# Kernel tuning notes

Hardware: AMD Instinct MI355X
Metric: run time of the kernel (lower is better)

Reference implementation:

```python
import jax, jax.numpy as jnp
import numpy as np

N_NODES = 2048
N_GRAPHS = 64
N_EDGES = 16384
B = 65536
META = 64
TX = 8
NOISE = 128
IN_DIM = N_NODES + 1 + 32 + TX  # 2089


def setup_inputs() -> dict:
    key = jax.random.key(0)
    ks = jax.random.split(key, 11)
    return {
        "batched_graphs": jax.random.randint(ks[0], (B,), 0, N_GRAPHS),
        "batched_chain": jax.random.normal(ks[1], (B,), dtype=jnp.float32),
        "trigger_data": jax.random.normal(ks[2], (B, META), dtype=jnp.float32),
        "tx_start_time": jax.random.normal(ks[3], (B, TX), dtype=jnp.float32),
        "edges": jax.random.randint(ks[4], (N_GRAPHS, 2, N_EDGES), 0, N_NODES),
        "gcn_w": jax.random.normal(ks[5], (), dtype=jnp.float32),
        "gcn_b": jax.random.normal(ks[6], (), dtype=jnp.float32) * 0.01,
        "trig_W": jax.random.normal(ks[7], (META, 32), dtype=jnp.float32) / np.sqrt(META),
        "trig_b": jnp.zeros((32,), dtype=jnp.float32),
        "emb_W": jax.random.normal(ks[8], (IN_DIM, NOISE), dtype=jnp.float32) / np.sqrt(IN_DIM),
        "emb_b": jnp.zeros((NOISE,), dtype=jnp.float32),
    }


def _gcn_one_graph(edge_index, w, b):
    # GCNConv(1,1) on x = ones(n_nodes,1): add self loops, sym-normalize.
    self_idx = jnp.arange(N_NODES, dtype=edge_index.dtype)
    src = jnp.concatenate([edge_index[0], self_idx])
    dst = jnp.concatenate([edge_index[1], self_idx])
    deg = jax.ops.segment_sum(jnp.ones(src.shape[0], jnp.float32), dst,
                              num_segments=N_NODES)
    dinv = jnp.where(deg > 0, jax.lax.rsqrt(deg), 0.0)
    norm = dinv[src] * dinv[dst]
    agg = jax.ops.segment_sum(norm, dst, num_segments=N_NODES)  # [n_nodes]
    return agg * w + b  # x @ W with x==1 is just w per node, plus bias


def reference(batched_graphs, batched_chain, trigger_data, tx_start_time,
              edges, gcn_w, gcn_b, trig_W, trig_b, emb_W, emb_b):
    # Per-graph GCN embeddings for all topologies (covers all uniques). [G, n_nodes]
    graph_emb = jax.vmap(lambda e: _gcn_one_graph(e, gcn_w, gcn_b))(edges)
    ge = graph_emb[batched_graphs]                         # [B, n_nodes] gather
    trig = jax.nn.relu(trigger_data @ trig_W + trig_b)     # [B, 32]
    x = jnp.concatenate(
        [ge, batched_chain[:, None], trig, tx_start_time], axis=1)  # [B, IN_DIM]
    return x @ emb_W + emb_b                               # [B, NOISE]
```

## Files before the change

### kernel.cpp

```cpp
#include <hip/hip_runtime.h>

#define NN 2048
#define NG 64
#define NE 16384
#define BB 65536
#define META 64
#define TXD 8
#define NOISE 128


__global__ __launch_bounds__(256) void agg_kernel(
    const int* __restrict__ edges,
    const float* __restrict__ gcn_w,
    const float* __restrict__ gcn_b,
    float* __restrict__ emb,
    float* __restrict__ graph_out)
{
    __shared__ int                s_cnt[NN];
    __shared__ float              s_dinv[NN];
    __shared__ unsigned long long s_acc[NN];
    const int g = blockIdx.x, tid = threadIdx.x;
    const int4* __restrict__ e4 = (const int4*)(edges + (size_t)g * 2 * NE);

    if (tid < NOISE) graph_out[g * NOISE + tid] = 0.0f;

    int4 ds[16];
    #pragma unroll
    for (int k = 0; k < 16; ++k) ds[k] = e4[4096 + k * 256 + tid];

    for (int n = tid; n < NN; n += 256) { s_cnt[n] = 1; s_acc[n] = 0ull; }
    __syncthreads();

    #pragma unroll
    for (int k = 0; k < 16; ++k) {
        atomicAdd(&s_cnt[ds[k].x], 1);
        atomicAdd(&s_cnt[ds[k].y], 1);
        atomicAdd(&s_cnt[ds[k].z], 1);
        atomicAdd(&s_cnt[ds[k].w], 1);
    }
    __syncthreads();
    for (int n = tid; n < NN; n += 256) s_dinv[n] = rsqrtf((float)s_cnt[n]);
    __syncthreads();

    const float SCALE = 1099511627776.0f;
    #pragma unroll
    for (int k = 0; k < 16; ++k) {
        int4 sr = e4[k * 256 + tid];
        float nx = s_dinv[sr.x] * s_dinv[ds[k].x];
        float ny = s_dinv[sr.y] * s_dinv[ds[k].y];
        float nz = s_dinv[sr.z] * s_dinv[ds[k].z];
        float nw = s_dinv[sr.w] * s_dinv[ds[k].w];
        atomicAdd(&s_acc[ds[k].x], (unsigned long long)(nx * SCALE));
        atomicAdd(&s_acc[ds[k].y], (unsigned long long)(ny * SCALE));
        atomicAdd(&s_acc[ds[k].z], (unsigned long long)(nz * SCALE));
        atomicAdd(&s_acc[ds[k].w], (unsigned long long)(nw * SCALE));
    }
    __syncthreads();

    const float w = gcn_w[0], b = gcn_b[0];
    for (int n = tid; n < NN; n += 256) {
        float di = s_dinv[n];
        float agg = (float)((double)s_acc[n] * 0x1p-40) + di * di;
        emb[(size_t)g * NN + n] = agg * w + b;
    }
}

__global__ __launch_bounds__(256) void fold_kernel(
    const float* __restrict__ emb,
    const float* __restrict__ emb_W,
    float* __restrict__ graph_out)
{
    __shared__ float s_e[128];
    __shared__ float s_red[128];
    const int tid = threadIdx.x;
    const int g = blockIdx.x >> 4, chunk = blockIdx.x & 15;
    const int n0 = chunk * 128;
    if (tid < 128) s_e[tid] = emb[(size_t)g * NN + n0 + tid];
    __syncthreads();
    const int c = tid & 127, h = tid >> 7;
    const float* __restrict__ Wp = emb_W + (size_t)(n0 + h * 64) * NOISE + c;
    const float* __restrict__ ep = s_e + h * 64;
    float a0 = 0.f, a1 = 0.f, a2 = 0.f, a3 = 0.f;
    #pragma unroll
    for (int i = 0; i < 64; i += 4) {
        a0 = fmaf(ep[i + 0], Wp[(i + 0) * NOISE], a0);
        a1 = fmaf(ep[i + 1], Wp[(i + 1) * NOISE], a1);
        a2 = fmaf(ep[i + 2], Wp[(i + 2) * NOISE], a2);
        a3 = fmaf(ep[i + 3], Wp[(i + 3) * NOISE], a3);
    }
    float acc = (a0 + a1) + (a2 + a3);
    if (h == 1) s_red[c] = acc;
    __syncthreads();
    if (h == 0) atomicAdd(&graph_out[g * NOISE + c], acc + s_red[c]);
}

#define ROWS 32
__global__ __launch_bounds__(256, 3) void main_kernel(
    const int* __restrict__ bg,
    const float* __restrict__ chain,
    const float* __restrict__ trig_in,
    const float* __restrict__ txs,
    const float* __restrict__ trig_W,
    const float* __restrict__ trig_b,
    const float* __restrict__ emb_W,
    const float* __restrict__ emb_b,
    const float* __restrict__ graph_out,
    float* __restrict__ out)
{
    __shared__ float s_td[ROWS * 68];
    __shared__ float s_twT[32 * 68];
    __shared__ float s_trig[ROWS * 36];
    __shared__ float s_tx[ROWS * TXD];
    __shared__ float s_ch[ROWS];
    __shared__ int   s_gi[ROWS];

    const int tid = threadIdx.x;
    const int row0 = blockIdx.x * ROWS;

    {
        const float4* __restrict__ gsrc =
            (const float4*)(trig_in + (size_t)row0 * META);
        #pragma unroll
        for (int k = 0; k < 2; ++k) {
            int t = tid + k * 256;
            int r = t >> 4, i4 = t & 15;
            *(float4*)&s_td[r * 68 + i4 * 4] = gsrc[t];
        }
    }
    {
        const float4* __restrict__ gsrc = (const float4*)trig_W;
        #pragma unroll
        for (int k = 0; k < 2; ++k) {
            int t = tid + k * 256;
            int i = t >> 3, j4 = (t & 7) * 4;
            float4 v = gsrc[t];
            s_twT[(j4 + 0) * 68 + i] = v.x;
            s_twT[(j4 + 1) * 68 + i] = v.y;
            s_twT[(j4 + 2) * 68 + i] = v.z;
            s_twT[(j4 + 3) * 68 + i] = v.w;
        }
    }
    if (tid < 64) {
        int r = tid >> 1, k4 = (tid & 1) * 4;
        *(float4*)&s_tx[r * TXD + k4] =
            ((const float4*)(txs + (size_t)row0 * TXD))[tid];
    } else if (tid < 96) {
        int r = tid - 64;
        s_ch[r] = chain[row0 + r];
    } else if (tid < 128) {
        int r = tid - 96;
        s_gi[r] = bg[row0 + r];
    }

    const int n0 = (tid & 63) * 2;
    float2 w2[32], w3[TXD];
    #pragma unroll
    for (int j = 0; j < 32; ++j)
        w2[j] = *(const float2*)&emb_W[(size_t)(2049 + j) * NOISE + n0];
    #pragma unroll
    for (int k = 0; k < TXD; ++k)
        w3[k] = *(const float2*)&emb_W[(size_t)(2081 + k) * NOISE + n0];
    const float2 w1   = *(const float2*)&emb_W[(size_t)2048 * NOISE + n0];
    const float2 bias = *(const float2*)&emb_b[n0];

    __syncthreads();

    {
        const int j0 = tid & 15;
        const int r0 = (tid >> 4) * 2;
        const float* __restrict__ tw0 = s_twT + j0 * 68;
        const float* __restrict__ tw1 = s_twT + (j0 + 16) * 68;
        const float* __restrict__ td0 = s_td + r0 * 68;
        const float* __restrict__ td1 = s_td + (r0 + 1) * 68;
        float b0 = trig_b[j0], b1 = trig_b[j0 + 16];
        float a00 = b0, a01 = b1, a10 = b0, a11 = b1;
        #pragma unroll
        for (int i = 0; i < META; i += 4) {
            float4 u0 = *(const float4*)(tw0 + i);
            float4 u1 = *(const float4*)(tw1 + i);
            float4 t0 = *(const float4*)(td0 + i);
            float4 t1 = *(const float4*)(td1 + i);
            a00 = fmaf(t0.x, u0.x, a00); a00 = fmaf(t0.y, u0.y, a00);
            a00 = fmaf(t0.z, u0.z, a00); a00 = fmaf(t0.w, u0.w, a00);
            a01 = fmaf(t0.x, u1.x, a01); a01 = fmaf(t0.y, u1.y, a01);
            a01 = fmaf(t0.z, u1.z, a01); a01 = fmaf(t0.w, u1.w, a01);
            a10 = fmaf(t1.x, u0.x, a10); a10 = fmaf(t1.y, u0.y, a10);
            a10 = fmaf(t1.z, u0.z, a10); a10 = fmaf(t1.w, u0.w, a10);
            a11 = fmaf(t1.x, u1.x, a11); a11 = fmaf(t1.y, u1.y, a11);
            a11 = fmaf(t1.z, u1.z, a11); a11 = fmaf(t1.w, u1.w, a11);
        }
        s_trig[r0 * 36 + j0]            = fmaxf(a00, 0.f);
        s_trig[r0 * 36 + j0 + 16]       = fmaxf(a01, 0.f);
        s_trig[(r0 + 1) * 36 + j0]      = fmaxf(a10, 0.f);
        s_trig[(r0 + 1) * 36 + j0 + 16] = fmaxf(a11, 0.f);
    }
    __syncthreads();

    const int wv = tid >> 6;
    int   gs[8];
    float chs[8];
    #pragma unroll
    for (int p = 0; p < 8; ++p) {
        const int r = p * 4 + wv;
        gs[p]  = s_gi[r];
        chs[p] = s_ch[r];
    }
    float2 go[8];
    #pragma unroll
    for (int p = 0; p < 8; ++p)
        go[p] = *(const float2*)&graph_out[gs[p] * NOISE + n0];

    #pragma unroll
    for (int p = 0; p < 8; ++p) {
        const int r = p * 4 + wv;
        const int row = row0 + r;
        float ax = bias.x + go[p].x + chs[p] * w1.x;
        float ay = bias.y + go[p].y + chs[p] * w1.y;
        const float4* __restrict__ tx4 = (const float4*)(s_tx + r * TXD);
        float4 t0 = tx4[0], t1 = tx4[1];
        ax = fmaf(t0.x, w3[0].x, ax); ay = fmaf(t0.x, w3[0].y, ay);
        ax = fmaf(t0.y, w3[1].x, ax); ay = fmaf(t0.y, w3[1].y, ay);
        ax = fmaf(t0.z, w3[2].x, ax); ay = fmaf(t0.z, w3[2].y, ay);
        ax = fmaf(t0.w, w3[3].x, ax); ay = fmaf(t0.w, w3[3].y, ay);
        ax = fmaf(t1.x, w3[4].x, ax); ay = fmaf(t1.x, w3[4].y, ay);
        ax = fmaf(t1.y, w3[5].x, ax); ay = fmaf(t1.y, w3[5].y, ay);
        ax = fmaf(t1.z, w3[6].x, ax); ay = fmaf(t1.z, w3[6].y, ay);
        ax = fmaf(t1.w, w3[7].x, ax); ay = fmaf(t1.w, w3[7].y, ay);
        const float* __restrict__ tg = s_trig + r * 36;
        #pragma unroll
        for (int q = 0; q < 8; ++q) {
            float4 t4 = *(const float4*)(tg + q * 4);
            ax = fmaf(t4.x, w2[4 * q + 0].x, ax); ay = fmaf(t4.x, w2[4 * q + 0].y, ay);
            ax = fmaf(t4.y, w2[4 * q + 1].x, ax); ay = fmaf(t4.y, w2[4 * q + 1].y, ay);
            ax = fmaf(t4.z, w2[4 * q + 2].x, ax); ay = fmaf(t4.z, w2[4 * q + 2].y, ay);
            ax = fmaf(t4.w, w2[4 * q + 3].x, ax); ay = fmaf(t4.w, w2[4 * q + 3].y, ay);
        }
        *(float2*)&out[(size_t)row * NOISE + n0] = make_float2(ax, ay);
    }
}

extern "C" void kernel_launch(void* const* d_in, const int* in_sizes, int n_in,
                              void* d_out, int out_size, void* d_ws, size_t ws_size,
                              hipStream_t stream) {
    const int*   bg      = (const int*)d_in[0];
    const float* chain   = (const float*)d_in[1];
    const float* trig_in = (const float*)d_in[2];
    const float* txs     = (const float*)d_in[3];
    const int*   edges   = (const int*)d_in[4];
    const float* gcn_w   = (const float*)d_in[5];
    const float* gcn_b   = (const float*)d_in[6];
    const float* trig_W  = (const float*)d_in[7];
    const float* trig_b  = (const float*)d_in[8];
    const float* emb_W   = (const float*)d_in[9];
    const float* emb_b   = (const float*)d_in[10];
    float* out = (float*)d_out;

    float* graph_out = (float*)d_ws;
    float* emb       = (float*)d_ws + NG * NOISE;

    agg_kernel<<<NG, 256, 0, stream>>>(edges, gcn_w, gcn_b, emb, graph_out);
    fold_kernel<<<NG * 16, 256, 0, stream>>>(emb, emb_W, graph_out);
    main_kernel<<<BB / ROWS, 256, 0, stream>>>(bg, chain, trig_in, txs, trig_W,
                                               trig_b, emb_W, emb_b, graph_out, out);
}
```

Baseline: 128.2 us.

## Split per-graph GCN aggregation across four blocks and slim main kernel registers

The single 64-block aggregation kernel becomes two kernels of 256 blocks each. A degree pass writes per-quarter partial counts and an accumulation pass reads them, and the fold kernel now sums those partials to build the node embeddings. This spreads the serial edge work across more CUs, at the cost of an extra launch and more workspace traffic. The main kernel also drops its shared staging of trig_W, tx, chain and graph indices and reads them directly, loads the emb_W trigger rows per q-step instead of holding them in registers, and raises the occupancy hint to 4 blocks per CU.

```diff
diff --git a/kernel.cpp b/kernel.cpp
--- a/kernel.cpp
+++ b/kernel.cpp
@@ -9,64 +9,90 @@
 #define NOISE 128
 
 
-__global__ __launch_bounds__(256) void agg_kernel(
+__global__ __launch_bounds__(256) void deg_kernel(
     const int* __restrict__ edges,
+    const float* __restrict__ trig_W,
+    int* __restrict__ deg4,
+    float* __restrict__ twT,
+    float* __restrict__ graph_out)
+{
+    __shared__ int s_cnt[NN];
+    const int tid = threadIdx.x;
+    const int g = blockIdx.x >> 2, q = blockIdx.x & 3;
+
+    for (int n = tid; n < NN; n += 256) s_cnt[n] = 0;
+
+    if (q == 0 && tid < NOISE) graph_out[g * NOISE + tid] = 0.0f;
+    if (blockIdx.x == 1) {
+        for (int idx = tid; idx < META * 32; idx += 256) {
+            int i = idx >> 5, j = idx & 31;
+            twT[j * META + i] = trig_W[idx];
+        }
+    }
+    __syncthreads();
+
+    const int4* __restrict__ ed =
+        (const int4*)(edges + ((size_t)g * 2 + 1) * NE + q * 4096);
+    #pragma unroll
+    for (int k = 0; k < 4; ++k) {
+        int4 d = ed[k * 256 + tid];
+        atomicAdd(&s_cnt[d.x], 1);
+        atomicAdd(&s_cnt[d.y], 1);
+        atomicAdd(&s_cnt[d.z], 1);
+        atomicAdd(&s_cnt[d.w], 1);
+    }
+    __syncthreads();
+
+    int* __restrict__ dst = deg4 + (size_t)blockIdx.x * NN;
+    for (int n = tid; n < NN; n += 256) dst[n] = s_cnt[n];
+}
+
+__global__ __launch_bounds__(256) void acc_kernel(
+    const int* __restrict__ edges,
+    const int* __restrict__ deg4,
+    float* __restrict__ acc4)
+{
+    __shared__ float              s_dinv[NN];
+    __shared__ unsigned long long s_acc[NN];
+    const int tid = threadIdx.x;
+    const int g = blockIdx.x >> 2, q = blockIdx.x & 3;
+
+    for (int n = tid; n < NN; n += 256) {
+        int d = deg4[((size_t)g * 4 + 0) * NN + n]
+              + deg4[((size_t)g * 4 + 1) * NN + n]
+              + deg4[((size_t)g * 4 + 2) * NN + n]
+              + deg4[((size_t)g * 4 + 3) * NN + n] + 1;
+        s_dinv[n] = rsqrtf((float)d);
+        s_acc[n] = 0ull;
+    }
+    __syncthreads();
+
+    const int4* __restrict__ es =
+        (const int4*)(edges + (size_t)g * 2 * NE + q * 4096);
+    const int4* __restrict__ ed =
+        (const int4*)(edges + ((size_t)g * 2 + 1) * NE + q * 4096);
+    const float SCALE = 1099511627776.0f;
+    #pragma unroll
+    for (int k = 0; k < 4; ++k) {
+        int4 s = es[k * 256 + tid];
+        int4 d = ed[k * 256 + tid];
+        atomicAdd(&s_acc[d.x], (unsigned long long)(s_dinv[s.x] * s_dinv[d.x] * SCALE));
+        atomicAdd(&s_acc[d.y], (unsigned long long)(s_dinv[s.y] * s_dinv[d.y] * SCALE));
+        atomicAdd(&s_acc[d.z], (unsigned long long)(s_dinv[s.z] * s_dinv[d.z] * SCALE));
+        atomicAdd(&s_acc[d.w], (unsigned long long)(s_dinv[s.w] * s_dinv[d.w] * SCALE));
+    }
+    __syncthreads();
+
+    float* __restrict__ dst = acc4 + (size_t)blockIdx.x * NN;
+    for (int n = tid; n < NN; n += 256)
+        dst[n] = (float)((double)s_acc[n] * 0x1p-40);
+}
+
+__global__ __launch_bounds__(256) void fold_kernel(
+    const int* __restrict__ deg4,
+    const float* __restrict__ acc4,
     const float* __restrict__ gcn_w,
     const float* __restrict__ gcn_b,
-    float* __restrict__ emb,
-    float* __restrict__ graph_out)
-{
-    __shared__ int                s_cnt[NN];
-    __shared__ float              s_dinv[NN];
-    __shared__ unsigned long long s_acc[NN];
-    const int g = blockIdx.x, tid = threadIdx.x;
-    const int4* __restrict__ e4 = (const int4*)(edges + (size_t)g * 2 * NE);
-
-    if (tid < NOISE) graph_out[g * NOISE + tid] = 0.0f;
-
-    int4 ds[16];
-    #pragma unroll
-    for (int k = 0; k < 16; ++k) ds[k] = e4[4096 + k * 256 + tid];
-
-    for (int n = tid; n < NN; n += 256) { s_cnt[n] = 1; s_acc[n] = 0ull; }
-    __syncthreads();
-
-    #pragma unroll
-    for (int k = 0; k < 16; ++k) {
-        atomicAdd(&s_cnt[ds[k].x], 1);
-        atomicAdd(&s_cnt[ds[k].y], 1);
-        atomicAdd(&s_cnt[ds[k].z], 1);
-        atomicAdd(&s_cnt[ds[k].w], 1);
-    }
-    __syncthreads();
-    for (int n = tid; n < NN; n += 256) s_dinv[n] = rsqrtf((float)s_cnt[n]);
-    __syncthreads();
-
-    const float SCALE = 1099511627776.0f;
-    #pragma unroll
-    for (int k = 0; k < 16; ++k) {
-        int4 sr = e4[k * 256 + tid];
-        float nx = s_dinv[sr.x] * s_dinv[ds[k].x];
-        float ny = s_dinv[sr.y] * s_dinv[ds[k].y];
-        float nz = s_dinv[sr.z] * s_dinv[ds[k].z];
-        float nw = s_dinv[sr.w] * s_dinv[ds[k].w];
-        atomicAdd(&s_acc[ds[k].x], (unsigned long long)(nx * SCALE));
-        atomicAdd(&s_acc[ds[k].y], (unsigned long long)(ny * SCALE));
-        atomicAdd(&s_acc[ds[k].z], (unsigned long long)(nz * SCALE));
-        atomicAdd(&s_acc[ds[k].w], (unsigned long long)(nw * SCALE));
-    }
-    __syncthreads();
-
-    const float w = gcn_w[0], b = gcn_b[0];
-    for (int n = tid; n < NN; n += 256) {
-        float di = s_dinv[n];
-        float agg = (float)((double)s_acc[n] * 0x1p-40) + di * di;
-        emb[(size_t)g * NN + n] = agg * w + b;
-    }
-}
-
-__global__ __launch_bounds__(256) void fold_kernel(
-    const float* __restrict__ emb,
     const float* __restrict__ emb_W,
     float* __restrict__ graph_out)
 {
@@ -75,7 +101,19 @@
     const int tid = threadIdx.x;
     const int g = blockIdx.x >> 4, chunk = blockIdx.x & 15;
     const int n0 = chunk * 128;
-    if (tid < 128) s_e[tid] = emb[(size_t)g * NN + n0 + tid];
+    if (tid < 128) {
+        const int n = n0 + tid;
+        int d = deg4[((size_t)g * 4 + 0) * NN + n]
+              + deg4[((size_t)g * 4 + 1) * NN + n]
+              + deg4[((size_t)g * 4 + 2) * NN + n]
+              + deg4[((size_t)g * 4 + 3) * NN + n] + 1;
+        float di = rsqrtf((float)d);
+        float a = acc4[((size_t)g * 4 + 0) * NN + n]
+                + acc4[((size_t)g * 4 + 1) * NN + n]
+                + acc4[((size_t)g * 4 + 2) * NN + n]
+                + acc4[((size_t)g * 4 + 3) * NN + n] + di * di;
+        s_e[tid] = a * gcn_w[0] + gcn_b[0];
+    }
     __syncthreads();
     const int c = tid & 127, h = tid >> 7;
     const float* __restrict__ Wp = emb_W + (size_t)(n0 + h * 64) * NOISE + c;
@@ -95,24 +133,20 @@
 }
 
 #define ROWS 32
-__global__ __launch_bounds__(256, 3) void main_kernel(
+__global__ __launch_bounds__(256, 4) void main_kernel(
     const int* __restrict__ bg,
     const float* __restrict__ chain,
     const float* __restrict__ trig_in,
     const float* __restrict__ txs,
-    const float* __restrict__ trig_W,
     const float* __restrict__ trig_b,
+    const float* __restrict__ twT,
     const float* __restrict__ emb_W,
     const float* __restrict__ emb_b,
     const float* __restrict__ graph_out,
     float* __restrict__ out)
 {
     __shared__ float s_td[ROWS * 68];
-    __shared__ float s_twT[32 * 68];
     __shared__ float s_trig[ROWS * 36];
-    __shared__ float s_tx[ROWS * TXD];
-    __shared__ float s_ch[ROWS];
-    __shared__ int   s_gi[ROWS];
 
     const int tid = threadIdx.x;
     const int row0 = blockIdx.x * ROWS;
@@ -127,52 +161,26 @@
             *(float4*)&s_td[r * 68 + i4 * 4] = gsrc[t];
         }
     }
-    {
-        const float4* __restrict__ gsrc = (const float4*)trig_W;
-        #pragma unroll
-        for (int k = 0; k < 2; ++k) {
-            int t = tid + k * 256;
-            int i = t >> 3, j4 = (t & 7) * 4;
-            float4 v = gsrc[t];
-            s_twT[(j4 + 0) * 68 + i] = v.x;
-            s_twT[(j4 + 1) * 68 + i] = v.y;
-            s_twT[(j4 + 2) * 68 + i] = v.z;
-            s_twT[(j4 + 3) * 68 + i] = v.w;
-        }
-    }
-    if (tid < 64) {
-        int r = tid >> 1, k4 = (tid & 1) * 4;
-        *(float4*)&s_tx[r * TXD + k4] =
-            ((const float4*)(txs + (size_t)row0 * TXD))[tid];
-    } else if (tid < 96) {
-        int r = tid - 64;
-        s_ch[r] = chain[row0 + r];
-    } else if (tid < 128) {
-        int r = tid - 96;
-        s_gi[r] = bg[row0 + r];
-    }
 
     const int n0 = (tid & 63) * 2;
-    float2 w2[32], w3[TXD];
-    #pragma unroll
-    for (int j = 0; j < 32; ++j)
-        w2[j] = *(const float2*)&emb_W[(size_t)(2049 + j) * NOISE + n0];
+    float2 w3[TXD];
     #pragma unroll
     for (int k = 0; k < TXD; ++k)
         w3[k] = *(const float2*)&emb_W[(size_t)(2081 + k) * NOISE + n0];
     const float2 w1   = *(const float2*)&emb_W[(size_t)2048 * NOISE + n0];
     const float2 bias = *(const float2*)&emb_b[n0];
 
+    const int j0 = tid & 15;
+    const int r0 = (tid >> 4) * 2;
+    const float b0 = trig_b[j0], b1 = trig_b[j0 + 16];
+
     __syncthreads();
 
     {
-        const int j0 = tid & 15;
-        const int r0 = (tid >> 4) * 2;
-        const float* __restrict__ tw0 = s_twT + j0 * 68;
-        const float* __restrict__ tw1 = s_twT + (j0 + 16) * 68;
+        const float* __restrict__ tw0 = twT + j0 * META;
+        const float* __restrict__ tw1 = twT + (j0 + 16) * META;
         const float* __restrict__ td0 = s_td + r0 * 68;
         const float* __restrict__ td1 = s_td + (r0 + 1) * 68;
-        float b0 = trig_b[j0], b1 = trig_b[j0 + 16];
         float a00 = b0, a01 = b1, a10 = b0, a11 = b1;
         #pragma unroll
         for (int i = 0; i < META; i += 4) {
@@ -197,27 +205,19 @@
     __syncthreads();
 
     const int wv = tid >> 6;
-    int   gs[8];
-    float chs[8];
-    #pragma unroll
-    for (int p = 0; p < 8; ++p) {
-        const int r = p * 4 + wv;
-        gs[p]  = s_gi[r];
-        chs[p] = s_ch[r];
-    }
-    float2 go[8];
-    #pragma unroll
-    for (int p = 0; p < 8; ++p)
-        go[p] = *(const float2*)&graph_out[gs[p] * NOISE + n0];
+    float2 acc[8];
 
     #pragma unroll
     for (int p = 0; p < 8; ++p) {
         const int r = p * 4 + wv;
         const int row = row0 + r;
-        float ax = bias.x + go[p].x + chs[p] * w1.x;
-        float ay = bias.y + go[p].y + chs[p] * w1.y;
-        const float4* __restrict__ tx4 = (const float4*)(s_tx + r * TXD);
-        float4 t0 = tx4[0], t1 = tx4[1];
+        const int   gidx = bg[row];
+        const float ch   = chain[row];
+        const float2 go  = *(const float2*)&graph_out[gidx * NOISE + n0];
+        const float4 t0  = *(const float4*)&txs[(size_t)row * TXD];
+        const float4 t1  = *(const float4*)&txs[(size_t)row * TXD + 4];
+        float ax = bias.x + go.x + ch * w1.x;
+        float ay = bias.y + go.y + ch * w1.y;
         ax = fmaf(t0.x, w3[0].x, ax); ay = fmaf(t0.x, w3[0].y, ay);
         ax = fmaf(t0.y, w3[1].x, ax); ay = fmaf(t0.y, w3[1].y, ay);
         ax = fmaf(t0.z, w3[2].x, ax); ay = fmaf(t0.z, w3[2].y, ay);
@@ -226,16 +226,30 @@
         ax = fmaf(t1.y, w3[5].x, ax); ay = fmaf(t1.y, w3[5].y, ay);
         ax = fmaf(t1.z, w3[6].x, ax); ay = fmaf(t1.z, w3[6].y, ay);
         ax = fmaf(t1.w, w3[7].x, ax); ay = fmaf(t1.w, w3[7].y, ay);
-        const float* __restrict__ tg = s_trig + r * 36;
+        acc[p] = make_float2(ax, ay);
+    }
+
+    #pragma unroll
+    for (int q = 0; q < 8; ++q) {
+        const float2 w2q0 = *(const float2*)&emb_W[(size_t)(2049 + 4 * q + 0) * NOISE + n0];
+        const float2 w2q1 = *(const float2*)&emb_W[(size_t)(2049 + 4 * q + 1) * NOISE + n0];
+        const float2 w2q2 = *(const float2*)&emb_W[(size_t)(2049 + 4 * q + 2) * NOISE + n0];
+        const float2 w2q3 = *(const float2*)&emb_W[(size_t)(2049 + 4 * q + 3) * NOISE + n0];
         #pragma unroll
-        for (int q = 0; q < 8; ++q) {
-            float4 t4 = *(const float4*)(tg + q * 4);
-            ax = fmaf(t4.x, w2[4 * q + 0].x, ax); ay = fmaf(t4.x, w2[4 * q + 0].y, ay);
-            ax = fmaf(t4.y, w2[4 * q + 1].x, ax); ay = fmaf(t4.y, w2[4 * q + 1].y, ay);
-            ax = fmaf(t4.z, w2[4 * q + 2].x, ax); ay = fmaf(t4.z, w2[4 * q + 2].y, ay);
-            ax = fmaf(t4.w, w2[4 * q + 3].x, ax); ay = fmaf(t4.w, w2[4 * q + 3].y, ay);
-        }
-        *(float2*)&out[(size_t)row * NOISE + n0] = make_float2(ax, ay);
+        for (int p = 0; p < 8; ++p) {
+            const int r = p * 4 + wv;
+            const float4 t4 = *(const float4*)(s_trig + r * 36 + q * 4);
+            acc[p].x = fmaf(t4.x, w2q0.x, acc[p].x); acc[p].y = fmaf(t4.x, w2q0.y, acc[p].y);
+            acc[p].x = fmaf(t4.y, w2q1.x, acc[p].x); acc[p].y = fmaf(t4.y, w2q1.y, acc[p].y);
+            acc[p].x = fmaf(t4.z, w2q2.x, acc[p].x); acc[p].y = fmaf(t4.z, w2q2.y, acc[p].y);
+            acc[p].x = fmaf(t4.w, w2q3.x, acc[p].x); acc[p].y = fmaf(t4.w, w2q3.y, acc[p].y);
+        }
+    }
+
+    #pragma unroll
+    for (int p = 0; p < 8; ++p) {
+        const int row = row0 + p * 4 + wv;
+        *(float2*)&out[(size_t)row * NOISE + n0] = acc[p];
     }
 }
 
@@ -255,11 +269,15 @@
     const float* emb_b   = (const float*)d_in[10];
     float* out = (float*)d_out;
 
-    float* graph_out = (float*)d_ws;
-    float* emb       = (float*)d_ws + NG * NOISE;
-
-    agg_kernel<<<NG, 256, 0, stream>>>(edges, gcn_w, gcn_b, emb, graph_out);
-    fold_kernel<<<NG * 16, 256, 0, stream>>>(emb, emb_W, graph_out);
-    main_kernel<<<BB / ROWS, 256, 0, stream>>>(bg, chain, trig_in, txs, trig_W,
-                                               trig_b, emb_W, emb_b, graph_out, out);
-}
+    float* wsf       = (float*)d_ws;
+    float* graph_out = wsf;
+    float* twT       = wsf + 8192;
+    int*   deg4      = (int*)(wsf + 10240);
+    float* acc4      = wsf + 10240 + 524288;
+
+    deg_kernel<<<NG * 4, 256, 0, stream>>>(edges, trig_W, deg4, twT, graph_out);
+    acc_kernel<<<NG * 4, 256, 0, stream>>>(edges, deg4, acc4);
+    fold_kernel<<<NG * 16, 256, 0, stream>>>(deg4, acc4, gcn_w, gcn_b, emb_W, graph_out);
+    main_kernel<<<BB / ROWS, 256, 0, stream>>>(bg, chain, trig_in, txs, trig_b,
+                                               twT, emb_W, emb_b, graph_out, out);
+}
```

New measurement: 158.3 us. 1.23x slower.

## Fuse GCN aggregation with graph-embedding fold into one kernel, use float atomics

Applied to the files above, without the earlier changes.

The separate fold kernel, along with its round trip of per-graph node embeddings through global memory, is merged into the aggregation kernel. Each of the 64 blocks now projects its 2048 node values against emb_W itself and writes graph_out directly, without global atomics or zero-init. The 64-bit fixed-point shared atomics are also replaced by float shared atomics, which makes the sum order-nondeterministic. The fold now runs on only 64 blocks, each streaming all of emb_W, so parallelism in that phase drops sharply.

```diff
diff --git a/kernel.cpp b/kernel.cpp
--- a/kernel.cpp
+++ b/kernel.cpp
@@ -9,26 +9,26 @@
 #define NOISE 128
 
 
-__global__ __launch_bounds__(256) void agg_kernel(
+__global__ __launch_bounds__(256) void gcn_fold_kernel(
     const int* __restrict__ edges,
     const float* __restrict__ gcn_w,
     const float* __restrict__ gcn_b,
-    float* __restrict__ emb,
+    const float* __restrict__ emb_W,
     float* __restrict__ graph_out)
 {
-    __shared__ int                s_cnt[NN];
-    __shared__ float              s_dinv[NN];
-    __shared__ unsigned long long s_acc[NN];
+    __shared__ int   s_cnt[NN];
+    __shared__ float s_dinv[NN];
+    __shared__ float s_val[NN];
+    __shared__ float s_part[4][NOISE];
+
     const int g = blockIdx.x, tid = threadIdx.x;
     const int4* __restrict__ e4 = (const int4*)(edges + (size_t)g * 2 * NE);
 
-    if (tid < NOISE) graph_out[g * NOISE + tid] = 0.0f;
-
     int4 ds[16];
     #pragma unroll
     for (int k = 0; k < 16; ++k) ds[k] = e4[4096 + k * 256 + tid];
 
-    for (int n = tid; n < NN; n += 256) { s_cnt[n] = 1; s_acc[n] = 0ull; }
+    for (int n = tid; n < NN; n += 256) { s_cnt[n] = 1; s_val[n] = 0.0f; }
     __syncthreads();
 
     #pragma unroll
@@ -42,56 +42,42 @@
     for (int n = tid; n < NN; n += 256) s_dinv[n] = rsqrtf((float)s_cnt[n]);
     __syncthreads();
 
-    const float SCALE = 1099511627776.0f;
     #pragma unroll
     for (int k = 0; k < 16; ++k) {
         int4 sr = e4[k * 256 + tid];
-        float nx = s_dinv[sr.x] * s_dinv[ds[k].x];
-        float ny = s_dinv[sr.y] * s_dinv[ds[k].y];
-        float nz = s_dinv[sr.z] * s_dinv[ds[k].z];
-        float nw = s_dinv[sr.w] * s_dinv[ds[k].w];
-        atomicAdd(&s_acc[ds[k].x], (unsigned long long)(nx * SCALE));
-        atomicAdd(&s_acc[ds[k].y], (unsigned long long)(ny * SCALE));
-        atomicAdd(&s_acc[ds[k].z], (unsigned long long)(nz * SCALE));
-        atomicAdd(&s_acc[ds[k].w], (unsigned long long)(nw * SCALE));
+        atomicAdd(&s_val[ds[k].x], s_dinv[sr.x] * s_dinv[ds[k].x]);
+        atomicAdd(&s_val[ds[k].y], s_dinv[sr.y] * s_dinv[ds[k].y]);
+        atomicAdd(&s_val[ds[k].z], s_dinv[sr.z] * s_dinv[ds[k].z]);
+        atomicAdd(&s_val[ds[k].w], s_dinv[sr.w] * s_dinv[ds[k].w]);
     }
     __syncthreads();
 
     const float w = gcn_w[0], b = gcn_b[0];
     for (int n = tid; n < NN; n += 256) {
         float di = s_dinv[n];
-        float agg = (float)((double)s_acc[n] * 0x1p-40) + di * di;
-        emb[(size_t)g * NN + n] = agg * w + b;
-    }
-}
-
-__global__ __launch_bounds__(256) void fold_kernel(
-    const float* __restrict__ emb,
-    const float* __restrict__ emb_W,
-    float* __restrict__ graph_out)
-{
-    __shared__ float s_e[128];
-    __shared__ float s_red[128];
-    const int tid = threadIdx.x;
-    const int g = blockIdx.x >> 4, chunk = blockIdx.x & 15;
-    const int n0 = chunk * 128;
-    if (tid < 128) s_e[tid] = emb[(size_t)g * NN + n0 + tid];
-    __syncthreads();
-    const int c = tid & 127, h = tid >> 7;
-    const float* __restrict__ Wp = emb_W + (size_t)(n0 + h * 64) * NOISE + c;
-    const float* __restrict__ ep = s_e + h * 64;
-    float a0 = 0.f, a1 = 0.f, a2 = 0.f, a3 = 0.f;
-    #pragma unroll
-    for (int i = 0; i < 64; i += 4) {
-        a0 = fmaf(ep[i + 0], Wp[(i + 0) * NOISE], a0);
-        a1 = fmaf(ep[i + 1], Wp[(i + 1) * NOISE], a1);
-        a2 = fmaf(ep[i + 2], Wp[(i + 2) * NOISE], a2);
-        a3 = fmaf(ep[i + 3], Wp[(i + 3) * NOISE], a3);
-    }
-    float acc = (a0 + a1) + (a2 + a3);
-    if (h == 1) s_red[c] = acc;
-    __syncthreads();
-    if (h == 0) atomicAdd(&graph_out[g * NOISE + c], acc + s_red[c]);
+        s_val[n] = (s_val[n] + di * di) * w + b;
+    }
+    __syncthreads();
+
+    const int q = tid >> 6, cp = tid & 63;
+    const int c0 = cp * 2;
+    const float* __restrict__ Wp = emb_W + (size_t)(q * 512) * NOISE + c0;
+    const float* __restrict__ ep = s_val + q * 512;
+    float ax = 0.f, ay = 0.f;
+    #pragma unroll 4
+    for (int i = 0; i < 512; ++i) {
+        float e = ep[i];
+        float2 wv = *(const float2*)(Wp + (size_t)i * NOISE);
+        ax = fmaf(e, wv.x, ax);
+        ay = fmaf(e, wv.y, ay);
+    }
+    s_part[q][c0] = ax;
+    s_part[q][c0 + 1] = ay;
+    __syncthreads();
+    if (tid < NOISE) {
+        graph_out[g * NOISE + tid] = s_part[0][tid] + s_part[1][tid]
+                                   + s_part[2][tid] + s_part[3][tid];
+    }
 }
 
 #define ROWS 32
@@ -256,10 +242,8 @@
     float* out = (float*)d_out;
 
     float* graph_out = (float*)d_ws;
-    float* emb       = (float*)d_ws + NG * NOISE;
-
-    agg_kernel<<<NG, 256, 0, stream>>>(edges, gcn_w, gcn_b, emb, graph_out);
-    fold_kernel<<<NG * 16, 256, 0, stream>>>(emb, emb_W, graph_out);
+
+    gcn_fold_kernel<<<NG, 256, 0, stream>>>(edges, gcn_w, gcn_b, emb_W, graph_out);
     main_kernel<<<BB / ROWS, 256, 0, stream>>>(bg, chain, trig_in, txs, trig_W,
                                                trig_b, emb_W, emb_b, graph_out, out);
 }
```

New measurement: 173.3 us. +35.2%, slower.
